# Performance work log

Hardware: AMD Instinct MI355X
Metric: run time of the kernel (lower is better)

The kernel has to match this reference:

```python
import jax, jax.numpy as jnp
import numpy as np

N_NODES = 100000
N_EDGES = 1600000
F_IN = 128
F_OUT = 64


def setup_inputs() -> dict:
    key = jax.random.key(0)
    k0, k1, k2, k3, k4, k5 = jax.random.split(key, 6)
    stdv = 1.0 / np.sqrt(F_OUT)
    x = jax.random.normal(k0, (N_NODES, F_IN), dtype=jnp.float32)
    edge_src = jax.random.randint(k1, (N_EDGES,), 0, N_NODES, dtype=jnp.int32)
    edge_dst = jax.random.randint(k2, (N_EDGES,), 0, N_NODES, dtype=jnp.int32)
    # normalized adjacency values (all positive, like D^-1/2 A D^-1/2 entries)
    edge_weight = jax.random.uniform(k3, (N_EDGES,), dtype=jnp.float32)
    weight = jax.random.uniform(k4, (F_IN, F_OUT), dtype=jnp.float32, minval=-stdv, maxval=stdv)
    bias = jax.random.uniform(k5, (F_OUT,), dtype=jnp.float32, minval=-stdv, maxval=stdv)
    return {"x": x, "edge_weight": edge_weight, "weight": weight, "bias": bias,
            "edge_src": edge_src, "edge_dst": edge_dst}


def reference(x, edge_weight, weight, bias, edge_src, edge_dst):
    # support = X @ W  -- dense GEMM [N, F_in] x [F_in, F_out]
    support = x @ weight
    # spmm(adj, support): adj in COO form; gather source rows, scale by edge value,
    # scatter-add into destination rows.
    msgs = support[edge_src] * edge_weight[:, None]          # [E, F_out]
    out = jax.ops.segment_sum(msgs, edge_dst, num_segments=x.shape[0])
    return out + bias
```

## Files before the change

kernel.cpp:

```cpp
#include <hip/hip_runtime.h>
#include <hip/hip_bf16.h>

#define F_IN 128
#define F_OUT 64
#define BUCKET_SHIFT 7
#define BUCKET_NODES 128
#define BUCKET_CAP 2880
#define CNT_STRIDE 16
#define NB_MAX 800
#define SCAT_CHUNK 16384
#define EPT 16
#define P1_GEMM_ROWS 128
#define LDK 136
#define SA_EPT 3

typedef __attribute__((ext_vector_type(8))) short bf16x8;
typedef __attribute__((ext_vector_type(4))) float f32x4;

__device__ inline short bf16_bits(float f) {
  __hip_bfloat16 h = __float2bfloat16(f);
  return *reinterpret_cast<short*>(&h);
}

union Phase1Smem {
  struct { short Bs[F_OUT][LDK]; } g;
  struct { int lhist[NB_MAX]; int lcur[NB_MAX]; } s;
};

__global__ __launch_bounds__(1024) void gcn_phase1_kernel(
    const float* __restrict__ x, const float* __restrict__ w,
    __hip_bfloat16* __restrict__ support,
    const int* __restrict__ esrc, const int* __restrict__ edst,
    const float* __restrict__ ew, int* __restrict__ bcount,
    int2* __restrict__ region, int n_nodes, int n_edges, int nb,
    int n_scat_blocks) {
  __shared__ Phase1Smem sm;
  const int tid = threadIdx.x;

  if ((int)blockIdx.x < n_scat_blocks) {
    const int e0 = blockIdx.x * SCAT_CHUNK;
    const int n_local = min(SCAT_CHUNK, n_edges - e0);

    for (int i = tid; i < nb; i += 1024) sm.s.lhist[i] = 0;
    __syncthreads();
    int dreg[EPT];
#pragma unroll
    for (int p = 0; p < EPT; ++p) {
      const int i = tid + p * 1024;
      dreg[p] = -1;
      if (i < n_local) {
        const int d = edst[e0 + i];
        dreg[p] = d;
        atomicAdd(&sm.s.lhist[d >> BUCKET_SHIFT], 1);
      }
    }
    __syncthreads();
    for (int b = tid; b < nb; b += 1024) {
      const int c = sm.s.lhist[b];
      const int rc = (c + 7) & ~7;
      sm.s.lcur[b] = rc ? atomicAdd(&bcount[b * CNT_STRIDE], rc) : 0;
    }
    __syncthreads();
#pragma unroll
    for (int p = 0; p < EPT; ++p) {
      const int i = tid + p * 1024;
      const int d = dreg[p];
      if (d >= 0) {
        const int b = d >> BUCKET_SHIFT;
        const int pos = atomicAdd(&sm.s.lcur[b], 1);
        if (pos < BUCKET_CAP) {
          region[(size_t)b * BUCKET_CAP + pos] = make_int2(
              (esrc[e0 + i] << BUCKET_SHIFT) | (d & (BUCKET_NODES - 1)),
              __float_as_int(ew[e0 + i]));
        }
      }
    }
    __syncthreads();
    for (int b = tid; b < nb; b += 1024) {
      const int c = sm.s.lhist[b];
      const int npad = (8 - (c & 7)) & 7;
      const int start = sm.s.lcur[b];
      for (int k = 0; k < npad; ++k) {
        const int pos = start + k;
        if (pos < BUCKET_CAP)
          region[(size_t)b * BUCKET_CAP + pos] =
              make_int2(pos & (BUCKET_NODES - 1), 0);
      }
    }
  } else {
    const int gbid = (int)blockIdx.x - n_scat_blocks;
    const int block_row = gbid * P1_GEMM_ROWS;

#pragma unroll
    for (int i = 0; i < F_IN * F_OUT / 1024; ++i) {
      const int idx = tid + i * 1024;
      sm.g.Bs[idx & 63][idx >> 6] = bf16_bits(w[idx]);
    }

    const int lane = tid & 63;
    const int wid = tid >> 6;
    const int wr0 = (wid >> 1) * 16;
    const int wc0 = (wid & 1) * 32;
    const int m = lane & 15;
    const int quad = lane >> 4;
    const int row = block_row + wr0 + m;

    bf16x8 afrag[4];
    if (row < n_nodes) {
      const float4* xr = (const float4*)(x + (size_t)row * F_IN);
#pragma unroll
      for (int ks = 0; ks < 4; ++ks) {
        const float4 v0 = xr[ks * 8 + quad * 2];
        const float4 v1 = xr[ks * 8 + quad * 2 + 1];
        bf16x8 a;
        a[0] = bf16_bits(v0.x); a[1] = bf16_bits(v0.y);
        a[2] = bf16_bits(v0.z); a[3] = bf16_bits(v0.w);
        a[4] = bf16_bits(v1.x); a[5] = bf16_bits(v1.y);
        a[6] = bf16_bits(v1.z); a[7] = bf16_bits(v1.w);
        afrag[ks] = a;
      }
    } else {
#pragma unroll
      for (int ks = 0; ks < 4; ++ks) afrag[ks] = (bf16x8)0;
    }
    __syncthreads();

    f32x4 acc0 = {0.f, 0.f, 0.f, 0.f};
    f32x4 acc1 = {0.f, 0.f, 0.f, 0.f};
#pragma unroll
    for (int ks = 0; ks < 4; ++ks) {
      const int ko = ks * 32 + quad * 8;
      const bf16x8 b0 = *(const bf16x8*)&sm.g.Bs[wc0 + m][ko];
      const bf16x8 b1 = *(const bf16x8*)&sm.g.Bs[wc0 + 16 + m][ko];
      acc0 = __builtin_amdgcn_mfma_f32_16x16x32_bf16(afrag[ks], b0, acc0, 0, 0, 0);
      acc1 = __builtin_amdgcn_mfma_f32_16x16x32_bf16(afrag[ks], b1, acc1, 0, 0, 0);
    }
#pragma unroll
    for (int r = 0; r < 4; ++r) {
      const int orow = block_row + wr0 + quad * 4 + r;
      if (orow < n_nodes) {
        __hip_bfloat16* op = support + (size_t)orow * F_OUT;
        op[wc0 + m]      = __float2bfloat16(acc0[r]);
        op[wc0 + 16 + m] = __float2bfloat16(acc1[r]);
      }
    }
  }
}

__global__ __launch_bounds__(1024) void gcn_sort_agg_kernel(
    const __hip_bfloat16* __restrict__ support,
    const int2* __restrict__ region, const int* __restrict__ bcount,
    const float* __restrict__ bias, float* __restrict__ out, int n_nodes) {
  __shared__ int2 outb[BUCKET_CAP];
  __shared__ int hist4[4][BUCKET_NODES];
  __shared__ int nbeg[BUCKET_NODES];
  __shared__ int lcur[BUCKET_NODES];
  const int b = blockIdx.x;
  const int tid = threadIdx.x;
  const int lane = tid & 63;
  const int hq = (tid >> 6) & 3;

  int cnt = bcount[b * CNT_STRIDE];
  cnt = (cnt < BUCKET_CAP ? cnt : BUCKET_CAP);
  const int2* reg = region + (size_t)b * BUCKET_CAP;

  for (int i = tid; i < 4 * BUCKET_NODES; i += 1024) ((int*)hist4)[i] = 0;
  __syncthreads();
  int2 ereg[SA_EPT];
#pragma unroll
  for (int p = 0; p < SA_EPT; ++p) {
    const int i = tid + p * 1024;
    ereg[p].x = -1;
    if (i < cnt) {
      ereg[p] = reg[i];
      atomicAdd(&hist4[hq][ereg[p].x & (BUCKET_NODES - 1)], 1);
    }
  }
  __syncthreads();
  if (tid < 64) {
    const int v0 = hist4[0][lane] + hist4[1][lane] + hist4[2][lane] +
                   hist4[3][lane];
    const int l1 = 64 + lane;
    const int v1 = hist4[0][l1] + hist4[1][l1] + hist4[2][l1] + hist4[3][l1];
    int s0 = v0;
#pragma unroll
    for (int off = 1; off < 64; off <<= 1) {
      const int t = __shfl_up(s0, off, 64);
      if (lane >= off) s0 += t;
    }
    const int tot0 = __shfl(s0, 63, 64);
    int s1 = v1;
#pragma unroll
    for (int off = 1; off < 64; off <<= 1) {
      const int t = __shfl_up(s1, off, 64);
      if (lane >= off) s1 += t;
    }
    s1 += tot0;
    nbeg[lane] = s0 - v0;
    nbeg[l1] = s1 - v1;
    lcur[lane] = s0 - v0;
    lcur[l1] = s1 - v1;
  }
  __syncthreads();
#pragma unroll
  for (int p = 0; p < SA_EPT; ++p) {
    if (ereg[p].x >= 0) {
      const int pos = atomicAdd(&lcur[ereg[p].x & (BUCKET_NODES - 1)], 1);
      outb[pos] = make_int2(ereg[p].x >> BUCKET_SHIFT, ereg[p].y);
    }
  }
  __syncthreads();

  const int wid = tid >> 6;
  const int r = lane >> 3;
  const int cg = lane & 7;
  const ushort* sup = (const ushort*)support;
  const float4 bb0 = *(const float4*)(bias + cg * 8);
  const float4 bb1 = *(const float4*)(bias + cg * 8 + 4);
  for (int nl = wid * 8; nl < wid * 8 + 8; ++nl) {
    const int g = (b << BUCKET_SHIFT) + nl;
    if (g >= n_nodes) break;
    const int s = nbeg[nl];
    const int e = lcur[nl];
    float acc0[8] = {0.f, 0.f, 0.f, 0.f, 0.f, 0.f, 0.f, 0.f};
    float acc1[8] = {0.f, 0.f, 0.f, 0.f, 0.f, 0.f, 0.f, 0.f};
    for (int j = s; j < e; j += 16) {
      const int jr0 = j + r;
      const int jr1 = j + 8 + r;
      const bool v0 = jr0 < e;
      const bool v1 = jr1 < e;
      const int2 m0 = outb[v0 ? jr0 : s];
      const int2 m1 = outb[v1 ? jr1 : s];
      const float w0 = v0 ? __int_as_float(m0.y) : 0.f;
      const float w1 = v1 ? __int_as_float(m1.y) : 0.f;
      const uint4 d0 = *(const uint4*)(sup + (size_t)m0.x * F_OUT + cg * 8);
      const uint4 d1 = *(const uint4*)(sup + (size_t)m1.x * F_OUT + cg * 8);
      acc0[0] = fmaf(__uint_as_float(d0.x << 16), w0, acc0[0]);
      acc0[1] = fmaf(__uint_as_float(d0.x & 0xffff0000u), w0, acc0[1]);
      acc0[2] = fmaf(__uint_as_float(d0.y << 16), w0, acc0[2]);
      acc0[3] = fmaf(__uint_as_float(d0.y & 0xffff0000u), w0, acc0[3]);
      acc0[4] = fmaf(__uint_as_float(d0.z << 16), w0, acc0[4]);
      acc0[5] = fmaf(__uint_as_float(d0.z & 0xffff0000u), w0, acc0[5]);
      acc0[6] = fmaf(__uint_as_float(d0.w << 16), w0, acc0[6]);
      acc0[7] = fmaf(__uint_as_float(d0.w & 0xffff0000u), w0, acc0[7]);
      acc1[0] = fmaf(__uint_as_float(d1.x << 16), w1, acc1[0]);
      acc1[1] = fmaf(__uint_as_float(d1.x & 0xffff0000u), w1, acc1[1]);
      acc1[2] = fmaf(__uint_as_float(d1.y << 16), w1, acc1[2]);
      acc1[3] = fmaf(__uint_as_float(d1.y & 0xffff0000u), w1, acc1[3]);
      acc1[4] = fmaf(__uint_as_float(d1.z << 16), w1, acc1[4]);
      acc1[5] = fmaf(__uint_as_float(d1.z & 0xffff0000u), w1, acc1[5]);
      acc1[6] = fmaf(__uint_as_float(d1.w << 16), w1, acc1[6]);
      acc1[7] = fmaf(__uint_as_float(d1.w & 0xffff0000u), w1, acc1[7]);
    }
#pragma unroll
    for (int i = 0; i < 8; ++i) {
      float v = acc0[i] + acc1[i];
      v += __shfl_xor(v, 8, 64);
      v += __shfl_xor(v, 16, 64);
      v += __shfl_xor(v, 32, 64);
      acc0[i] = v;
    }
    if (r == 0) {
      float* op = out + (size_t)g * F_OUT + cg * 8;
      float4 o0, o1;
      o0.x = acc0[0] + bb0.x; o0.y = acc0[1] + bb0.y;
      o0.z = acc0[2] + bb0.z; o0.w = acc0[3] + bb0.w;
      o1.x = acc0[4] + bb1.x; o1.y = acc0[5] + bb1.y;
      o1.z = acc0[6] + bb1.z; o1.w = acc0[7] + bb1.w;
      *(float4*)op = o0;
      *(float4*)(op + 4) = o1;
    }
  }
}

extern "C" void kernel_launch(void* const* d_in, const int* in_sizes, int n_in,
                              void* d_out, int out_size, void* d_ws, size_t ws_size,
                              hipStream_t stream) {
  const float* x    = (const float*)d_in[0];
  const float* ew   = (const float*)d_in[1];
  const float* w    = (const float*)d_in[2];
  const float* bias = (const float*)d_in[3];
  const int*   esrc = (const int*)d_in[4];
  const int*   edst = (const int*)d_in[5];
  float* out = (float*)d_out;

  const int n_nodes = in_sizes[0] / F_IN;
  const int n_edges = in_sizes[4];
  const int nb = (n_nodes + BUCKET_NODES - 1) >> BUCKET_SHIFT;

  char* ws = (char*)d_ws;
  size_t off = 0;
  auto alloc = [&](size_t bytes) {
    size_t o = off;
    off += (bytes + 255) / 256 * 256;
    return o;
  };
  const size_t off_bcount  = alloc((size_t)nb * CNT_STRIDE * sizeof(int));
  const size_t off_region  = alloc((size_t)nb * BUCKET_CAP * sizeof(int2));
  const size_t off_support = alloc((size_t)n_nodes * F_OUT * sizeof(__hip_bfloat16));
  (void)off_support;

  int*  bcount = (int*)(ws + off_bcount);
  int2* region = (int2*)(ws + off_region);
  __hip_bfloat16* support = (__hip_bfloat16*)(ws + off_support);

  const int scat_blocks = (n_edges + SCAT_CHUNK - 1) / SCAT_CHUNK;
  const int gemm_blocks = (n_nodes + P1_GEMM_ROWS - 1) / P1_GEMM_ROWS;

  hipMemsetAsync(bcount, 0, (size_t)nb * CNT_STRIDE * sizeof(int), stream);
  gcn_phase1_kernel<<<scat_blocks + gemm_blocks, 1024, 0, stream>>>(
      x, w, support, esrc, edst, ew, bcount, region, n_nodes, n_edges, nb,
      scat_blocks);
  gcn_sort_agg_kernel<<<nb, 1024, 0, stream>>>(support, region, bcount, bias,
                                               out, n_nodes);
}
```

Measured before the change: 194.9 us.

## Stage bucket scatter in shared memory for coalesced region writes

The edge-bucketing pass now computes a block-local prefix scan of the per-bucket histogram. It sorts each chunk's edges into a shared-memory buffer grouped by bucket, then writes them to the global region in thread order, so consecutive threads hit consecutive addresses within a bucket. The aim is to replace scattered global stores with mostly contiguous ones. The chunk size drops to 4096 edges so the staging buffers fit in shared memory, which means more blocks and more global atomics on the bucket counters. The per-chunk padding of each bucket to a multiple of 8 is also removed; this is only safe if the consumer kernel does not rely on that padding.

After: 182.8 us. 6.2% less time.

```diff
diff --git a/kernel.cpp b/kernel.cpp
--- a/kernel.cpp
+++ b/kernel.cpp
@@ -8,8 +8,8 @@
 #define BUCKET_CAP 2880
 #define CNT_STRIDE 16
 #define NB_MAX 800
-#define SCAT_CHUNK 16384
-#define EPT 16
+#define SCAT_CHUNK 4096
+#define EPT 4
 #define P1_GEMM_ROWS 128
 #define LDK 136
 #define SA_EPT 3
@@ -24,7 +24,15 @@
 
 union Phase1Smem {
   struct { short Bs[F_OUT][LDK]; } g;
-  struct { int lhist[NB_MAX]; int lcur[NB_MAX]; } s;
+  struct {
+    int2 ebuf[SCAT_CHUNK];
+    int  gaddr[SCAT_CHUNK];
+    int  lhist[NB_MAX];
+    int  lbeg[NB_MAX];
+    int  lcur[NB_MAX];
+    int  gbase[NB_MAX];
+    int  wtot[16];
+  } s;
 };
 
 __global__ __launch_bounds__(1024) void gcn_phase1_kernel(
@@ -36,6 +44,8 @@
     int n_scat_blocks) {
   __shared__ Phase1Smem sm;
   const int tid = threadIdx.x;
+  const int lane = tid & 63;
+  const int wid = tid >> 6;
 
   if ((int)blockIdx.x < n_scat_blocks) {
     const int e0 = blockIdx.x * SCAT_CHUNK;
@@ -55,10 +65,31 @@
       }
     }
     __syncthreads();
-    for (int b = tid; b < nb; b += 1024) {
-      const int c = sm.s.lhist[b];
-      const int rc = (c + 7) & ~7;
-      sm.s.lcur[b] = rc ? atomicAdd(&bcount[b * CNT_STRIDE], rc) : 0;
+    const int c = (tid < nb) ? sm.s.lhist[tid] : 0;
+    int sc = c;
+#pragma unroll
+    for (int off = 1; off < 64; off <<= 1) {
+      const int t = __shfl_up(sc, off, 64);
+      if (lane >= off) sc += t;
+    }
+    if (lane == 63) sm.s.wtot[wid] = sc;
+    __syncthreads();
+    if (wid == 0) {
+      const int wv = (lane < 16) ? sm.s.wtot[lane] : 0;
+      int ws = wv;
+#pragma unroll
+      for (int off = 1; off < 16; off <<= 1) {
+        const int t = __shfl_up(ws, off, 64);
+        if (lane >= off) ws += t;
+      }
+      if (lane < 16) sm.s.wtot[lane] = ws - wv;
+    }
+    __syncthreads();
+    if (tid < nb) {
+      const int beg = (sc - c) + sm.s.wtot[wid];
+      sm.s.lbeg[tid] = beg;
+      sm.s.lcur[tid] = beg;
+      sm.s.gbase[tid] = c ? atomicAdd(&bcount[tid * CNT_STRIDE], c) : 0;
     }
     __syncthreads();
 #pragma unroll
@@ -68,23 +99,20 @@
       if (d >= 0) {
         const int b = d >> BUCKET_SHIFT;
         const int pos = atomicAdd(&sm.s.lcur[b], 1);
-        if (pos < BUCKET_CAP) {
-          region[(size_t)b * BUCKET_CAP + pos] = make_int2(
-              (esrc[e0 + i] << BUCKET_SHIFT) | (d & (BUCKET_NODES - 1)),
-              __float_as_int(ew[e0 + i]));
-        }
-      }
-    }
-    __syncthreads();
-    for (int b = tid; b < nb; b += 1024) {
-      const int c = sm.s.lhist[b];
-      const int npad = (8 - (c & 7)) & 7;
-      const int start = sm.s.lcur[b];
-      for (int k = 0; k < npad; ++k) {
-        const int pos = start + k;
-        if (pos < BUCKET_CAP)
-          region[(size_t)b * BUCKET_CAP + pos] =
-              make_int2(pos & (BUCKET_NODES - 1), 0);
+        const int slot = sm.s.gbase[b] + (pos - sm.s.lbeg[b]);
+        sm.s.ebuf[pos] = make_int2(
+            (esrc[e0 + i] << BUCKET_SHIFT) | (d & (BUCKET_NODES - 1)),
+            __float_as_int(ew[e0 + i]));
+        sm.s.gaddr[pos] = (slot < BUCKET_CAP) ? b * BUCKET_CAP + slot : -1;
+      }
+    }
+    __syncthreads();
+#pragma unroll
+    for (int p = 0; p < EPT; ++p) {
+      const int i = tid + p * 1024;
+      if (i < n_local) {
+        const int ga = sm.s.gaddr[i];
+        if (ga >= 0) region[ga] = sm.s.ebuf[i];
       }
     }
   } else {
@@ -97,8 +125,6 @@
       sm.g.Bs[idx & 63][idx >> 6] = bf16_bits(w[idx]);
     }
 
-    const int lane = tid & 63;
-    const int wid = tid >> 6;
     const int wr0 = (wid >> 1) * 16;
     const int wc0 = (wid & 1) * 32;
     const int m = lane & 15;
```
